# Kernel tuning notes

Hardware: AMD Instinct MI355X
Metric: run time of the kernel (lower is better)

## Reference

```python
import jax, jax.numpy as jnp
import numpy as np

P_X, P_H, P_L, P_VT, P_ET, B = 512, 1024, 4, 512, 256, 512
IN_DIM = P_X + 2 * P_H  # concat([x, prev_time_h, prev_layer_h])


def setup_inputs() -> dict:
    key = jax.random.key(0)
    ks = jax.random.split(key, 10)
    sc_in = 1.0 / np.sqrt(IN_DIM)
    sc_lh = 1.0 / np.sqrt(P_L * P_H)
    return {
        "input_x": jax.random.normal(ks[0], (B, P_X), jnp.float32),
        "h_prev": jax.random.normal(ks[1], (P_L, B, P_H), jnp.float32),
        "c_prev": jax.random.normal(ks[2], (P_L, B, P_H), jnp.float32),
        # stacked gate weights: [L, 4 gates (i,f,o,s), h, in_dim]
        "Wg": jax.random.uniform(ks[3], (P_L, 4, P_H, IN_DIM), jnp.float32, -sc_in, sc_in),
        "bg": jax.random.uniform(ks[4], (P_L, 4, P_H), jnp.float32, -sc_in, sc_in),
        "W_y": jax.random.uniform(ks[5], (P_VT, P_L * P_H), jnp.float32, -sc_lh, sc_lh),
        "b_y": jax.random.uniform(ks[6], (P_VT,), jnp.float32, -sc_lh, sc_lh),
        "W_E": jax.random.uniform(ks[7], (P_ET, P_L * P_H), jnp.float32, -sc_lh, sc_lh),
        "b_E": jax.random.uniform(ks[8], (P_ET,), jnp.float32, -sc_lh, sc_lh),
    }


def _controller(input_x, h_prev, c_prev, Wg, bg):
    prev_layer = jnp.zeros((input_x.shape[0], P_H), input_x.dtype)
    hiddens = []
    for i in range(P_L):  # loop over small fixed layer count
        z = jnp.concatenate([input_x, h_prev[i], prev_layer], axis=-1)  # [B, IN_DIM]
        g = jnp.einsum("bd,ghd->bgh", z, Wg[i]) + bg[i]  # [B, 4, H], one fused GEMM
        i_g = jax.nn.sigmoid(g[:, 0])
        f_g = jax.nn.sigmoid(g[:, 1])
        o_g = jax.nn.sigmoid(g[:, 2])
        s_g = jnp.tanh(g[:, 3])
        c_new = f_g * c_prev[i] + i_g * s_g
        h_new = o_g * jnp.tanh(c_new)
        hiddens.append(h_new)
        prev_layer = h_new
    return jnp.concatenate(hiddens, axis=-1)  # [B, L*H]


def reference(input_x, h_prev, c_prev, Wg, bg, W_y, b_y, W_E, b_E):
    hidden = _controller(input_x, h_prev, c_prev, Wg, bg)
    output = hidden @ W_y.T + b_y      # [B, v_t]
    interface = hidden @ W_E.T + b_E   # [B, E_t]
    return (output, interface)
```

## Files before the change

kernel.cpp:

```cpp
#include <hip/hip_runtime.h>


typedef short    shortx8  __attribute__((ext_vector_type(8)));
typedef float    floatx16 __attribute__((ext_vector_type(16)));

__device__ __forceinline__ unsigned int f2bf1(float x) {
  unsigned int u = __float_as_uint(x);
  return (u + 0x7fffu + ((u >> 16) & 1u)) >> 16;
}
__device__ __forceinline__ unsigned int f2bf2(float lo, float hi) {
  return f2bf1(lo) | (f2bf1(hi) << 16);
}

__global__ __launch_bounds__(256) void prep_z(const float* __restrict__ x,
                                              const float* __restrict__ hp,
                                              unsigned short* __restrict__ z) {
  const int layer = blockIdx.y;
  const int idx   = blockIdx.x * 256 + threadIdx.x;
  const int b     = idx / 320;
  const int kk    = (idx - b * 320) * 8;
  float v[8];
  if (kk < 512) {
    const float* s = x + (size_t)b * 512 + kk;
#pragma unroll
    for (int i = 0; i < 8; ++i) v[i] = s[i];
  } else if (kk < 1536) {
    const float* s = hp + ((size_t)layer * 512 + b) * 1024 + (kk - 512);
#pragma unroll
    for (int i = 0; i < 8; ++i) v[i] = s[i];
  } else {
    if (layer != 0) return;
#pragma unroll
    for (int i = 0; i < 8; ++i) v[i] = 0.f;
  }
  uint4 o;
  o.x = f2bf2(v[0], v[1]); o.y = f2bf2(v[2], v[3]);
  o.z = f2bf2(v[4], v[5]); o.w = f2bf2(v[6], v[7]);
  *(uint4*)(z + ((size_t)layer * 512 + b) * 2560 + kk) = o;
}

__global__ __launch_bounds__(256) void gemm_bt_split(
    const unsigned short* __restrict__ A, int lda,
    const float* __restrict__ B0, int nb0,
    const float* __restrict__ B1,
    float* __restrict__ Cp, int ldc, int mtotal, int ktiles) {
  __shared__ __align__(16) unsigned short As[128 * 64];
  __shared__ __align__(16) unsigned short Bs[128 * 64];
  const int tid  = threadIdx.x;
  const int lane = tid & 63;
  const int wave = tid >> 6;
  const int mbase = blockIdx.z * 128;
  const int nt    = blockIdx.y;
  const int nbase = nt * 128;
  const float* Bb = (nt < nb0) ? (B0 + (size_t)nbase * lda)
                               : (B1 + (size_t)(nbase - nb0 * 128) * lda);
  const int k0 = blockIdx.x * (ktiles * 64);

  floatx16 acc[2][2];
#pragma unroll
  for (int a = 0; a < 2; ++a)
#pragma unroll
    for (int bb = 0; bb < 2; ++bb)
#pragma unroll
      for (int r = 0; r < 16; ++r) acc[a][bb][r] = 0.f;

  const int wm = (wave >> 1) * 64;
  const int wn = (wave & 1) * 64;
  const int arow = wave * 8 + (lane >> 3);
  const int akg  = lane & 7;
  const unsigned short* Ab = A + (size_t)mbase * lda;

  for (int kt = 0; kt < ktiles; ++kt) {
    const int kg = k0 + kt * 64;
#pragma unroll
    for (int r = 0; r < 4; ++r) {
      const int row = arow + r * 32;
      const uint4 av = *(const uint4*)(Ab + (size_t)row * lda + kg + akg * 8);
      *(uint4*)(As + row * 64 + ((akg ^ (row & 7)) * 8)) = av;
    }
#pragma unroll
    for (int j = 0; j < 8; ++j) {
      const int idx = j * 256 + tid;
      const int n   = idx >> 4;
      const int kc  = (idx & 15) * 4;
      const float4 bv = *(const float4*)(Bb + (size_t)n * lda + kg + kc);
      uint2 pk;
      pk.x = f2bf2(bv.x, bv.y);
      pk.y = f2bf2(bv.z, bv.w);
      const int g    = kc >> 3;
      const int half = kc & 4;
      *(uint2*)(Bs + n * 64 + ((g ^ (n & 7)) * 8) + half) = pk;
    }
    __syncthreads();
#pragma unroll
    for (int ks = 0; ks < 4; ++ks) {
      const int gb = ks * 2 + (lane >> 5);
      shortx8 af[2], bf[2];
#pragma unroll
      for (int sm = 0; sm < 2; ++sm) {
        const int row = wm + sm * 32 + (lane & 31);
        af[sm] = *(const shortx8*)(As + row * 64 + ((gb ^ (row & 7)) * 8));
      }
#pragma unroll
      for (int sn = 0; sn < 2; ++sn) {
        const int row = wn + sn * 32 + (lane & 31);
        bf[sn] = *(const shortx8*)(Bs + row * 64 + ((gb ^ (row & 7)) * 8));
      }
#pragma unroll
      for (int sm = 0; sm < 2; ++sm)
#pragma unroll
        for (int sn = 0; sn < 2; ++sn)
          acc[sm][sn] = __builtin_amdgcn_mfma_f32_32x32x16_bf16(
              af[sm], bf[sn], acc[sm][sn], 0, 0, 0);
    }
    __syncthreads();
  }

  float* Co = Cp + (size_t)blockIdx.x * mtotal * ldc;
#pragma unroll
  for (int sm = 0; sm < 2; ++sm)
#pragma unroll
    for (int sn = 0; sn < 2; ++sn) {
      const int col = nbase + wn + sn * 32 + (lane & 31);
#pragma unroll
      for (int r = 0; r < 16; ++r) {
        const int row = mbase + wm + sm * 32 +
                        ((r & 3) + 8 * (r >> 2) + 4 * (lane >> 5));
        Co[(size_t)row * ldc + col] = acc[sm][sn][r];
      }
    }
}

__global__ __launch_bounds__(256) void lstm_pointwise(
    const float* __restrict__ gp, const float* __restrict__ bg_l,
    const float* __restrict__ cp_l, unsigned short* __restrict__ hidden,
    unsigned short* __restrict__ znext, int layer) {
  const int idx = (blockIdx.x * 256 + threadIdx.x) * 4;
  const int b = idx >> 10;
  const int h = idx & 1023;
  const float* g0 = gp + (size_t)b * 4096;
  const float* g1 = gp + (size_t)512 * 4096 + (size_t)b * 4096;
  float4 vi = *(const float4*)(g0 + h);
  float4 vf = *(const float4*)(g0 + 1024 + h);
  float4 vo = *(const float4*)(g0 + 2048 + h);
  float4 vs = *(const float4*)(g0 + 3072 + h);
  const float4 wi = *(const float4*)(g1 + h);
  const float4 wf = *(const float4*)(g1 + 1024 + h);
  const float4 wo = *(const float4*)(g1 + 2048 + h);
  const float4 ws = *(const float4*)(g1 + 3072 + h);
  const float4 bi = *(const float4*)(bg_l + h);
  const float4 bff = *(const float4*)(bg_l + 1024 + h);
  const float4 bo = *(const float4*)(bg_l + 2048 + h);
  const float4 bs = *(const float4*)(bg_l + 3072 + h);
  const float4 cp = *(const float4*)(cp_l + (size_t)b * 1024 + h);

  float gi[4] = {vi.x + wi.x + bi.x, vi.y + wi.y + bi.y,
                 vi.z + wi.z + bi.z, vi.w + wi.w + bi.w};
  float gf[4] = {vf.x + wf.x + bff.x, vf.y + wf.y + bff.y,
                 vf.z + wf.z + bff.z, vf.w + wf.w + bff.w};
  float go[4] = {vo.x + wo.x + bo.x, vo.y + wo.y + bo.y,
                 vo.z + wo.z + bo.z, vo.w + wo.w + bo.w};
  float gs[4] = {vs.x + ws.x + bs.x, vs.y + ws.y + bs.y,
                 vs.z + ws.z + bs.z, vs.w + ws.w + bs.w};
  const float cc[4] = {cp.x, cp.y, cp.z, cp.w};
  float hn[4];
#pragma unroll
  for (int j = 0; j < 4; ++j) {
    const float ig = 1.f / (1.f + __expf(-gi[j]));
    const float fg = 1.f / (1.f + __expf(-gf[j]));
    const float og = 1.f / (1.f + __expf(-go[j]));
    const float sg = 1.f - 2.f / (__expf(2.f * gs[j]) + 1.f);
    const float c  = fg * cc[j] + ig * sg;
    const float tc = 1.f - 2.f / (__expf(2.f * c) + 1.f);
    hn[j] = og * tc;
  }
  uint2 o;
  o.x = f2bf2(hn[0], hn[1]);
  o.y = f2bf2(hn[2], hn[3]);
  *(uint2*)(hidden + (size_t)b * 4096 + layer * 1024 + h) = o;
  if (znext) *(uint2*)(znext + (size_t)b * 2560 + 1536 + h) = o;
}

__global__ __launch_bounds__(256) void head_reduce(
    const float* __restrict__ hp, const float* __restrict__ b_y,
    const float* __restrict__ b_E, float* __restrict__ out) {
  const int n = blockIdx.x * 256 + threadIdx.x;
  const int b = blockIdx.y;
  float s = 0.f;
#pragma unroll
  for (int ks = 0; ks < 8; ++ks) s += hp[(size_t)ks * 512 * 768 + (size_t)b * 768 + n];
  if (n < 512)
    out[(size_t)b * 512 + n] = s + b_y[n];
  else
    out[(size_t)512 * 512 + (size_t)b * 256 + (n - 512)] = s + b_E[n - 512];
}

extern "C" void kernel_launch(void* const* d_in, const int* in_sizes, int n_in,
                              void* d_out, int out_size, void* d_ws, size_t ws_size,
                              hipStream_t stream) {
  const float* x      = (const float*)d_in[0];
  const float* h_prev = (const float*)d_in[1];
  const float* c_prev = (const float*)d_in[2];
  const float* Wg     = (const float*)d_in[3];
  const float* bg     = (const float*)d_in[4];
  const float* W_y    = (const float*)d_in[5];
  const float* b_y    = (const float*)d_in[6];
  const float* W_E    = (const float*)d_in[7];
  const float* b_E    = (const float*)d_in[8];

  char* ws = (char*)d_ws;
  unsigned short* z      = (unsigned short*)(ws + 0);
  unsigned short* hidden = (unsigned short*)(ws + 10485760);
  float*          gpart  = (float*)(ws + 14680064);

  prep_z<<<dim3(640, 4), 256, 0, stream>>>(x, h_prev, z);

  for (int l = 0; l < 4; ++l) {
    gemm_bt_split<<<dim3(2, 32, 4), 256, 0, stream>>>(
        z + (size_t)l * 512 * 2560, 2560,
        Wg + (size_t)l * 4 * 1024 * 2560, 32, nullptr,
        gpart, 4096, 512, 20);
    lstm_pointwise<<<512, 256, 0, stream>>>(
        gpart, bg + (size_t)l * 4096, c_prev + (size_t)l * 512 * 1024,
        hidden, (l < 3) ? (z + (size_t)(l + 1) * 512 * 2560) : nullptr, l);
  }

  gemm_bt_split<<<dim3(8, 6, 4), 256, 0, stream>>>(
      hidden, 4096, W_y, 4, W_E, gpart, 768, 512, 8);
  head_reduce<<<dim3(3, 512), 256, 0, stream>>>(gpart, b_y, b_E, (float*)d_out);
}
```

Baseline: 451.1 us.

## Hoist non-recurrent gate GEMM for all layers, fuse recurrent GEMM with cell

The x and h_prev parts of the gate GEMM (K=1536) are now computed for all four layers in one batched launch with the bias folded in. Only the prev-layer part (K=1024) stays sequential, in a kernel that fuses the LSTM cell math into its epilogue by tiling gate columns so each block holds all four gates for 16 hidden units. This drops the redundant zero-padded K for layer 0 and removes the split-K partials and separate pointwise launches. All GEMMs also gain register-prefetched LDS double buffering. The cost is an extra fp32 gate buffer in memory and small-N tiles in the sequential kernel.

```diff
diff --git a/kernel.cpp b/kernel.cpp
--- a/kernel.cpp
+++ b/kernel.cpp
@@ -11,112 +11,347 @@
 __device__ __forceinline__ unsigned int f2bf2(float lo, float hi) {
   return f2bf1(lo) | (f2bf1(hi) << 16);
 }
-
-__global__ __launch_bounds__(256) void prep_z(const float* __restrict__ x,
-                                              const float* __restrict__ hp,
-                                              unsigned short* __restrict__ z) {
-  const int layer = blockIdx.y;
-  const int idx   = blockIdx.x * 256 + threadIdx.x;
-  const int b     = idx / 320;
-  const int kk    = (idx - b * 320) * 8;
+__device__ __forceinline__ float sigm(float x) { return 1.f / (1.f + __expf(-x)); }
+__device__ __forceinline__ float tanh_(float x) { return 1.f - 2.f / (__expf(2.f * x) + 1.f); }
+
+__global__ __launch_bounds__(256) void prep_a0(const float* __restrict__ x,
+                                               const float* __restrict__ hp,
+                                               unsigned short* __restrict__ A0) {
+  const int l   = blockIdx.y;
+  const int idx = blockIdx.x * 256 + threadIdx.x;
+  const int b   = idx / 192;
+  const int kk  = (idx - b * 192) * 8;
   float v[8];
   if (kk < 512) {
     const float* s = x + (size_t)b * 512 + kk;
 #pragma unroll
     for (int i = 0; i < 8; ++i) v[i] = s[i];
-  } else if (kk < 1536) {
-    const float* s = hp + ((size_t)layer * 512 + b) * 1024 + (kk - 512);
+  } else {
+    const float* s = hp + ((size_t)l * 512 + b) * 1024 + (kk - 512);
 #pragma unroll
     for (int i = 0; i < 8; ++i) v[i] = s[i];
-  } else {
-    if (layer != 0) return;
-#pragma unroll
-    for (int i = 0; i < 8; ++i) v[i] = 0.f;
   }
   uint4 o;
   o.x = f2bf2(v[0], v[1]); o.y = f2bf2(v[2], v[3]);
   o.z = f2bf2(v[4], v[5]); o.w = f2bf2(v[6], v[7]);
-  *(uint4*)(z + ((size_t)layer * 512 + b) * 2560 + kk) = o;
-}
-
-__global__ __launch_bounds__(256) void gemm_bt_split(
-    const unsigned short* __restrict__ A, int lda,
-    const float* __restrict__ B0, int nb0,
-    const float* __restrict__ B1,
-    float* __restrict__ Cp, int ldc, int mtotal, int ktiles) {
-  __shared__ __align__(16) unsigned short As[128 * 64];
-  __shared__ __align__(16) unsigned short Bs[128 * 64];
-  const int tid  = threadIdx.x;
-  const int lane = tid & 63;
-  const int wave = tid >> 6;
+  *(uint4*)(A0 + ((size_t)l * 512 + b) * 1536 + kk) = o;
+}
+
+__global__ __launch_bounds__(256, 2) void gemm_gates(
+    const unsigned short* __restrict__ A0, const float* __restrict__ Wg,
+    const float* __restrict__ bg, float* __restrict__ G) {
+  __shared__ __align__(16) unsigned short As[2][128 * 64];
+  __shared__ __align__(16) unsigned short Bs[2][128 * 64];
+  const int tid = threadIdx.x, lane = tid & 63, wave = tid >> 6;
+  const int mbase = blockIdx.x * 128;
+  const int nbase = blockIdx.y * 128;
+  const int l     = blockIdx.z;
+  const unsigned short* Ab = A0 + ((size_t)l * 512 + mbase) * 1536;
+  const float*          Bb = Wg + (size_t)l * 4096 * 2560 + (size_t)nbase * 2560;
+  const int arow = wave * 8 + (lane >> 3);
+  const int akg  = lane & 7;
+
+  uint4  apf[4];
+  float4 bpf[8];
+  auto loadT = [&](int kt) {
+    const int kg = kt * 64;
+#pragma unroll
+    for (int r = 0; r < 4; ++r)
+      apf[r] = *(const uint4*)(Ab + (size_t)(arow + r * 32) * 1536 + kg + akg * 8);
+#pragma unroll
+    for (int j = 0; j < 8; ++j) {
+      const int idx = j * 256 + tid;
+      bpf[j] = *(const float4*)(Bb + (size_t)(idx >> 4) * 2560 + kg + (idx & 15) * 4);
+    }
+  };
+  auto storeT = [&](int buf) {
+#pragma unroll
+    for (int r = 0; r < 4; ++r) {
+      const int row = arow + r * 32;
+      *(uint4*)(&As[buf][row * 64 + ((akg ^ (row & 7)) * 8)]) = apf[r];
+    }
+#pragma unroll
+    for (int j = 0; j < 8; ++j) {
+      const int idx = j * 256 + tid;
+      const int n = idx >> 4, kc = (idx & 15) * 4;
+      uint2 pk;
+      pk.x = f2bf2(bpf[j].x, bpf[j].y);
+      pk.y = f2bf2(bpf[j].z, bpf[j].w);
+      *(uint2*)(&Bs[buf][n * 64 + (((kc >> 3) ^ (n & 7)) * 8) + (kc & 4)]) = pk;
+    }
+  };
+
+  floatx16 acc[2][2];
+#pragma unroll
+  for (int a = 0; a < 2; ++a)
+#pragma unroll
+    for (int b2 = 0; b2 < 2; ++b2)
+#pragma unroll
+      for (int r = 0; r < 16; ++r) acc[a][b2][r] = 0.f;
+
+  const int wm = (wave >> 1) * 64, wn = (wave & 1) * 64;
+  loadT(0);
+  storeT(0);
+  __syncthreads();
+  for (int kt = 0; kt < 24; ++kt) {
+    if (kt + 1 < 24) loadT(kt + 1);
+    const int cb = kt & 1;
+#pragma unroll
+    for (int ks = 0; ks < 4; ++ks) {
+      const int gb = ks * 2 + (lane >> 5);
+      shortx8 af[2], bfv[2];
+#pragma unroll
+      for (int sm = 0; sm < 2; ++sm) {
+        const int row = wm + sm * 32 + (lane & 31);
+        af[sm] = *(const shortx8*)(&As[cb][row * 64 + ((gb ^ (row & 7)) * 8)]);
+      }
+#pragma unroll
+      for (int sn = 0; sn < 2; ++sn) {
+        const int row = wn + sn * 32 + (lane & 31);
+        bfv[sn] = *(const shortx8*)(&Bs[cb][row * 64 + ((gb ^ (row & 7)) * 8)]);
+      }
+#pragma unroll
+      for (int sm = 0; sm < 2; ++sm)
+#pragma unroll
+        for (int sn = 0; sn < 2; ++sn)
+          acc[sm][sn] = __builtin_amdgcn_mfma_f32_32x32x16_bf16(
+              af[sm], bfv[sn], acc[sm][sn], 0, 0, 0);
+    }
+    if (kt + 1 < 24) storeT((kt + 1) & 1);
+    __syncthreads();
+  }
+
+  const float* bgl = bg + (size_t)l * 4096;
+  float* Gl = G + ((size_t)l * 512 + mbase) * 4096;
+#pragma unroll
+  for (int sm = 0; sm < 2; ++sm)
+#pragma unroll
+    for (int sn = 0; sn < 2; ++sn) {
+      const int col = nbase + wn + sn * 32 + (lane & 31);
+      const float bias = bgl[col];
+#pragma unroll
+      for (int r = 0; r < 16; ++r) {
+        const int row = wm + sm * 32 + ((r & 3) + 8 * (r >> 2) + 4 * (lane >> 5));
+        Gl[(size_t)row * 4096 + col] = acc[sm][sn][r] + bias;
+      }
+    }
+}
+
+__global__ __launch_bounds__(256) void cell0(const float* __restrict__ G,
+                                             const float* __restrict__ cp_l,
+                                             unsigned short* __restrict__ hidden) {
+  const int idx = (blockIdx.x * 256 + threadIdx.x) * 4;
+  const int b = idx >> 10, h = idx & 1023;
+  const float* g0 = G + (size_t)b * 4096;
+  const float4 vi = *(const float4*)(g0 + h);
+  const float4 vf = *(const float4*)(g0 + 1024 + h);
+  const float4 vo = *(const float4*)(g0 + 2048 + h);
+  const float4 vs = *(const float4*)(g0 + 3072 + h);
+  const float4 cp = *(const float4*)(cp_l + (size_t)b * 1024 + h);
+  const float gi[4] = {vi.x, vi.y, vi.z, vi.w};
+  const float gf[4] = {vf.x, vf.y, vf.z, vf.w};
+  const float go[4] = {vo.x, vo.y, vo.z, vo.w};
+  const float gs[4] = {vs.x, vs.y, vs.z, vs.w};
+  const float cc[4] = {cp.x, cp.y, cp.z, cp.w};
+  float hn[4];
+#pragma unroll
+  for (int j = 0; j < 4; ++j) {
+    const float c = sigm(gf[j]) * cc[j] + sigm(gi[j]) * tanh_(gs[j]);
+    hn[j] = sigm(go[j]) * tanh_(c);
+  }
+  uint2 o;
+  o.x = f2bf2(hn[0], hn[1]);
+  o.y = f2bf2(hn[2], hn[3]);
+  *(uint2*)(hidden + (size_t)b * 4096 + h) = o;
+}
+
+__global__ __launch_bounds__(512, 2) void gemm_seq_cell(
+    const unsigned short* __restrict__ hidden_ro, const float* __restrict__ Wg,
+    const float* __restrict__ G, const float* __restrict__ c_prev,
+    unsigned short* __restrict__ hidden_w, int l) {
+  __shared__ __align__(16) unsigned char raw[49152];
+  unsigned short* As = (unsigned short*)raw;
+  unsigned short* Bs = (unsigned short*)(raw + 32768);
+  float*          Gex = (float*)raw;
+  const int tid = threadIdx.x, lane = tid & 63, wave = tid >> 6;
+  const int mbase = blockIdx.x * 128;
+  const int h0    = blockIdx.y * 16;
+  const unsigned short* Ab = hidden_ro + (size_t)(l - 1) * 1024;
+  const float*          Bl = Wg + (size_t)l * 4096 * 2560 + 1536;
+
+  uint4  apf[2];
+  float4 bpf[2];
+  auto loadT = [&](int kt) {
+    const int kg = kt * 64;
+#pragma unroll
+    for (int r = 0; r < 2; ++r) {
+      const int row = (tid >> 3) + r * 64;
+      apf[r] = *(const uint4*)(Ab + (size_t)(mbase + row) * 4096 + kg + (tid & 7) * 8);
+    }
+#pragma unroll
+    for (int j = 0; j < 2; ++j) {
+      const int idx = j * 512 + tid;
+      const int nl = idx >> 4, kc = (idx & 15) * 4;
+      const int grow = (nl >> 4) * 1024 + h0 + (nl & 15);
+      bpf[j] = *(const float4*)(Bl + (size_t)grow * 2560 + kg + kc);
+    }
+  };
+  auto storeT = [&](int buf) {
+#pragma unroll
+    for (int r = 0; r < 2; ++r) {
+      const int row = (tid >> 3) + r * 64;
+      *(uint4*)(&As[buf * 8192 + row * 64 + (((tid & 7) ^ (row & 7)) * 8)]) = apf[r];
+    }
+#pragma unroll
+    for (int j = 0; j < 2; ++j) {
+      const int idx = j * 512 + tid;
+      const int nl = idx >> 4, kc = (idx & 15) * 4;
+      uint2 pk;
+      pk.x = f2bf2(bpf[j].x, bpf[j].y);
+      pk.y = f2bf2(bpf[j].z, bpf[j].w);
+      *(uint2*)(&Bs[buf * 4096 + nl * 64 + (((kc >> 3) ^ (nl & 7)) * 8) + (kc & 4)]) = pk;
+    }
+  };
+
+  floatx16 acc;
+#pragma unroll
+  for (int r = 0; r < 16; ++r) acc[r] = 0.f;
+  const int wm = (wave & 3) * 32, wn = (wave >> 2) * 32;
+
+  loadT(0);
+  storeT(0);
+  __syncthreads();
+  for (int kt = 0; kt < 16; ++kt) {
+    if (kt + 1 < 16) loadT(kt + 1);
+    const int cb = kt & 1;
+    const int rowa = wm + (lane & 31);
+    const int rowb = wn + (lane & 31);
+#pragma unroll
+    for (int ks = 0; ks < 4; ++ks) {
+      const int gb = ks * 2 + (lane >> 5);
+      const shortx8 af = *(const shortx8*)(&As[cb * 8192 + rowa * 64 + ((gb ^ (rowa & 7)) * 8)]);
+      const shortx8 bfv = *(const shortx8*)(&Bs[cb * 4096 + rowb * 64 + ((gb ^ (rowb & 7)) * 8)]);
+      acc = __builtin_amdgcn_mfma_f32_32x32x16_bf16(af, bfv, acc, 0, 0, 0);
+    }
+    if (kt + 1 < 16) storeT((kt + 1) & 1);
+    __syncthreads();
+  }
+
+  {
+    const int col = wn + (lane & 31);
+#pragma unroll
+    for (int r = 0; r < 16; ++r) {
+      const int row = wm + ((r & 3) + 8 * (r >> 2) + 4 * (lane >> 5));
+      Gex[row * 65 + col] = acc[r];
+    }
+  }
+  __syncthreads();
+
+  const int hh = tid & 15, q = tid >> 4;
+#pragma unroll
+  for (int bi = 0; bi < 4; ++bi) {
+    const int bl = bi * 32 + q;
+    const int b  = mbase + bl;
+    const int hg = h0 + hh;
+    const float* Gb = G + ((size_t)l * 512 + b) * 4096;
+    float gv[4];
+#pragma unroll
+    for (int g = 0; g < 4; ++g)
+      gv[g] = Gex[bl * 65 + g * 16 + hh] + Gb[g * 1024 + hg];
+    const float c_old = c_prev[((size_t)l * 512 + b) * 1024 + hg];
+    const float c  = sigm(gv[1]) * c_old + sigm(gv[0]) * tanh_(gv[3]);
+    const float hn = sigm(gv[2]) * tanh_(c);
+    hidden_w[(size_t)b * 4096 + l * 1024 + hg] = (unsigned short)f2bf1(hn);
+  }
+}
+
+__global__ __launch_bounds__(256) void gemm_heads(
+    const unsigned short* __restrict__ A, const float* __restrict__ Wy,
+    const float* __restrict__ WE, float* __restrict__ Cp) {
+  __shared__ __align__(16) unsigned short As[2][128 * 64];
+  __shared__ __align__(16) unsigned short Bs[2][128 * 64];
+  const int tid = threadIdx.x, lane = tid & 63, wave = tid >> 6;
   const int mbase = blockIdx.z * 128;
   const int nt    = blockIdx.y;
   const int nbase = nt * 128;
-  const float* Bb = (nt < nb0) ? (B0 + (size_t)nbase * lda)
-                               : (B1 + (size_t)(nbase - nb0 * 128) * lda);
-  const int k0 = blockIdx.x * (ktiles * 64);
-
-  floatx16 acc[2][2];
-#pragma unroll
-  for (int a = 0; a < 2; ++a)
-#pragma unroll
-    for (int bb = 0; bb < 2; ++bb)
-#pragma unroll
-      for (int r = 0; r < 16; ++r) acc[a][bb][r] = 0.f;
-
-  const int wm = (wave >> 1) * 64;
-  const int wn = (wave & 1) * 64;
+  const float* Bb = (nt < 4) ? (Wy + (size_t)nbase * 4096)
+                             : (WE + (size_t)(nbase - 512) * 4096);
+  const int k0 = blockIdx.x * 512;
+  const unsigned short* Ab = A + (size_t)mbase * 4096;
   const int arow = wave * 8 + (lane >> 3);
   const int akg  = lane & 7;
-  const unsigned short* Ab = A + (size_t)mbase * lda;
-
-  for (int kt = 0; kt < ktiles; ++kt) {
+
+  uint4  apf[4];
+  float4 bpf[8];
+  auto loadT = [&](int kt) {
     const int kg = k0 + kt * 64;
+#pragma unroll
+    for (int r = 0; r < 4; ++r)
+      apf[r] = *(const uint4*)(Ab + (size_t)(arow + r * 32) * 4096 + kg + akg * 8);
+#pragma unroll
+    for (int j = 0; j < 8; ++j) {
+      const int idx = j * 256 + tid;
+      bpf[j] = *(const float4*)(Bb + (size_t)(idx >> 4) * 4096 + kg + (idx & 15) * 4);
+    }
+  };
+  auto storeT = [&](int buf) {
 #pragma unroll
     for (int r = 0; r < 4; ++r) {
       const int row = arow + r * 32;
-      const uint4 av = *(const uint4*)(Ab + (size_t)row * lda + kg + akg * 8);
-      *(uint4*)(As + row * 64 + ((akg ^ (row & 7)) * 8)) = av;
+      *(uint4*)(&As[buf][row * 64 + ((akg ^ (row & 7)) * 8)]) = apf[r];
     }
 #pragma unroll
     for (int j = 0; j < 8; ++j) {
       const int idx = j * 256 + tid;
-      const int n   = idx >> 4;
-      const int kc  = (idx & 15) * 4;
-      const float4 bv = *(const float4*)(Bb + (size_t)n * lda + kg + kc);
+      const int n = idx >> 4, kc = (idx & 15) * 4;
       uint2 pk;
-      pk.x = f2bf2(bv.x, bv.y);
-      pk.y = f2bf2(bv.z, bv.w);
-      const int g    = kc >> 3;
-      const int half = kc & 4;
-      *(uint2*)(Bs + n * 64 + ((g ^ (n & 7)) * 8) + half) = pk;
-    }
-    __syncthreads();
+      pk.x = f2bf2(bpf[j].x, bpf[j].y);
+      pk.y = f2bf2(bpf[j].z, bpf[j].w);
+      *(uint2*)(&Bs[buf][n * 64 + (((kc >> 3) ^ (n & 7)) * 8) + (kc & 4)]) = pk;
+    }
+  };
+
+  floatx16 acc[2][2];
+#pragma unroll
+  for (int a = 0; a < 2; ++a)
+#pragma unroll
+    for (int b2 = 0; b2 < 2; ++b2)
+#pragma unroll
+      for (int r = 0; r < 16; ++r) acc[a][b2][r] = 0.f;
+  const int wm = (wave >> 1) * 64, wn = (wave & 1) * 64;
+
+  loadT(0);
+  storeT(0);
+  __syncthreads();
+  for (int kt = 0; kt < 8; ++kt) {
+    if (kt + 1 < 8) loadT(kt + 1);
+    const int cb = kt & 1;
 #pragma unroll
     for (int ks = 0; ks < 4; ++ks) {
       const int gb = ks * 2 + (lane >> 5);
-      shortx8 af[2], bf[2];
+      shortx8 af[2], bfv[2];
 #pragma unroll
       for (int sm = 0; sm < 2; ++sm) {
         const int row = wm + sm * 32 + (lane & 31);
-        af[sm] = *(const shortx8*)(As + row * 64 + ((gb ^ (row & 7)) * 8));
+        af[sm] = *(const shortx8*)(&As[cb][row * 64 + ((gb ^ (row & 7)) * 8)]);
       }
 #pragma unroll
       for (int sn = 0; sn < 2; ++sn) {
         const int row = wn + sn * 32 + (lane & 31);
-        bf[sn] = *(const shortx8*)(Bs + row * 64 + ((gb ^ (row & 7)) * 8));
+        bfv[sn] = *(const shortx8*)(&Bs[cb][row * 64 + ((gb ^ (row & 7)) * 8)]);
       }
 #pragma unroll
       for (int sm = 0; sm < 2; ++sm)
 #pragma unroll
         for (int sn = 0; sn < 2; ++sn)
           acc[sm][sn] = __builtin_amdgcn_mfma_f32_32x32x16_bf16(
-              af[sm], bf[sn], acc[sm][sn], 0, 0, 0);
-    }
+              af[sm], bfv[sn], acc[sm][sn], 0, 0, 0);
+    }
+    if (kt + 1 < 8) storeT((kt + 1) & 1);
     __syncthreads();
   }
 
-  float* Co = Cp + (size_t)blockIdx.x * mtotal * ldc;
+  float* Co = Cp + (size_t)blockIdx.x * 512 * 768;
 #pragma unroll
   for (int sm = 0; sm < 2; ++sm)
 #pragma unroll
@@ -126,59 +361,9 @@
       for (int r = 0; r < 16; ++r) {
         const int row = mbase + wm + sm * 32 +
                         ((r & 3) + 8 * (r >> 2) + 4 * (lane >> 5));
-        Co[(size_t)row * ldc + col] = acc[sm][sn][r];
-      }
-    }
-}
-
-__global__ __launch_bounds__(256) void lstm_pointwise(
-    const float* __restrict__ gp, const float* __restrict__ bg_l,
-    const float* __restrict__ cp_l, unsigned short* __restrict__ hidden,
-    unsigned short* __restrict__ znext, int layer) {
-  const int idx = (blockIdx.x * 256 + threadIdx.x) * 4;
-  const int b = idx >> 10;
-  const int h = idx & 1023;
-  const float* g0 = gp + (size_t)b * 4096;
-  const float* g1 = gp + (size_t)512 * 4096 + (size_t)b * 4096;
-  float4 vi = *(const float4*)(g0 + h);
-  float4 vf = *(const float4*)(g0 + 1024 + h);
-  float4 vo = *(const float4*)(g0 + 2048 + h);
-  float4 vs = *(const float4*)(g0 + 3072 + h);
-  const float4 wi = *(const float4*)(g1 + h);
-  const float4 wf = *(const float4*)(g1 + 1024 + h);
-  const float4 wo = *(const float4*)(g1 + 2048 + h);
-  const float4 ws = *(const float4*)(g1 + 3072 + h);
-  const float4 bi = *(const float4*)(bg_l + h);
-  const float4 bff = *(const float4*)(bg_l + 1024 + h);
-  const float4 bo = *(const float4*)(bg_l + 2048 + h);
-  const float4 bs = *(const float4*)(bg_l + 3072 + h);
-  const float4 cp = *(const float4*)(cp_l + (size_t)b * 1024 + h);
-
-  float gi[4] = {vi.x + wi.x + bi.x, vi.y + wi.y + bi.y,
-                 vi.z + wi.z + bi.z, vi.w + wi.w + bi.w};
-  float gf[4] = {vf.x + wf.x + bff.x, vf.y + wf.y + bff.y,
-                 vf.z + wf.z + bff.z, vf.w + wf.w + bff.w};
-  float go[4] = {vo.x + wo.x + bo.x, vo.y + wo.y + bo.y,
-                 vo.z + wo.z + bo.z, vo.w + wo.w + bo.w};
-  float gs[4] = {vs.x + ws.x + bs.x, vs.y + ws.y + bs.y,
-                 vs.z + ws.z + bs.z, vs.w + ws.w + bs.w};
-  const float cc[4] = {cp.x, cp.y, cp.z, cp.w};
-  float hn[4];
-#pragma unroll
-  for (int j = 0; j < 4; ++j) {
-    const float ig = 1.f / (1.f + __expf(-gi[j]));
-    const float fg = 1.f / (1.f + __expf(-gf[j]));
-    const float og = 1.f / (1.f + __expf(-go[j]));
-    const float sg = 1.f - 2.f / (__expf(2.f * gs[j]) + 1.f);
-    const float c  = fg * cc[j] + ig * sg;
-    const float tc = 1.f - 2.f / (__expf(2.f * c) + 1.f);
-    hn[j] = og * tc;
-  }
-  uint2 o;
-  o.x = f2bf2(hn[0], hn[1]);
-  o.y = f2bf2(hn[2], hn[3]);
-  *(uint2*)(hidden + (size_t)b * 4096 + layer * 1024 + h) = o;
-  if (znext) *(uint2*)(znext + (size_t)b * 2560 + 1536 + h) = o;
+        Co[(size_t)row * 768 + col] = acc[sm][sn][r];
+      }
+    }
 }
 
 __global__ __launch_bounds__(256) void head_reduce(
@@ -188,7 +373,8 @@
   const int b = blockIdx.y;
   float s = 0.f;
 #pragma unroll
-  for (int ks = 0; ks < 8; ++ks) s += hp[(size_t)ks * 512 * 768 + (size_t)b * 768 + n];
+  for (int ks = 0; ks < 8; ++ks)
+    s += hp[(size_t)ks * 512 * 768 + (size_t)b * 768 + n];
   if (n < 512)
     out[(size_t)b * 512 + n] = s + b_y[n];
   else
@@ -209,23 +395,17 @@
   const float* b_E    = (const float*)d_in[8];
 
   char* ws = (char*)d_ws;
-  unsigned short* z      = (unsigned short*)(ws + 0);
-  unsigned short* hidden = (unsigned short*)(ws + 10485760);
-  float*          gpart  = (float*)(ws + 14680064);
-
-  prep_z<<<dim3(640, 4), 256, 0, stream>>>(x, h_prev, z);
-
-  for (int l = 0; l < 4; ++l) {
-    gemm_bt_split<<<dim3(2, 32, 4), 256, 0, stream>>>(
-        z + (size_t)l * 512 * 2560, 2560,
-        Wg + (size_t)l * 4 * 1024 * 2560, 32, nullptr,
-        gpart, 4096, 512, 20);
-    lstm_pointwise<<<512, 256, 0, stream>>>(
-        gpart, bg + (size_t)l * 4096, c_prev + (size_t)l * 512 * 1024,
-        hidden, (l < 3) ? (z + (size_t)(l + 1) * 512 * 2560) : nullptr, l);
-  }
-
-  gemm_bt_split<<<dim3(8, 6, 4), 256, 0, stream>>>(
-      hidden, 4096, W_y, 4, W_E, gpart, 768, 512, 8);
-  head_reduce<<<dim3(3, 512), 256, 0, stream>>>(gpart, b_y, b_E, (float*)d_out);
-}
+  unsigned short* A0     = (unsigned short*)(ws + 0);
+  float*          G      = (float*)(ws + 6291456);
+  unsigned short* hidden = (unsigned short*)(ws + 39845888);
+  float*          hpart  = (float*)(ws + 44040192);
+
+  prep_a0<<<dim3(384, 4), 256, 0, stream>>>(x, h_prev, A0);
+  gemm_gates<<<dim3(4, 32, 4), 256, 0, stream>>>(A0, Wg, bg, G);
+  cell0<<<512, 256, 0, stream>>>(G, c_prev, hidden);
+  for (int l = 1; l < 4; ++l)
+    gemm_seq_cell<<<dim3(4, 64), 512, 0, stream>>>(hidden, Wg, G, c_prev,
+                                                   hidden, l);
+  gemm_heads<<<dim3(8, 6, 4), 256, 0, stream>>>(hidden, W_y, W_E, hpart);
+  head_reduce<<<dim3(3, 512), 256, 0, stream>>>(hpart, b_y, b_E, (float*)d_out);
+}
```

Measured after the change: 404.9 us. 1.11x faster.
